# Kernel tuning notes

Hardware: AMD Instinct MI355X
Metric: run time of the kernel (lower is better)

## Reference

```python
import jax, jax.numpy as jnp
import numpy as np

HIDDEN = 1024
HEADS = 8
HEAD = HIDDEN // HEADS
EPS = 1e-5


def _gammas():
    lo = np.log(1.0 / 512.0)
    hi = np.log(1.0 / 32.0)
    lin = np.linspace(lo, hi, HEADS)
    return jnp.asarray(1.0 - np.exp(lin), dtype=jnp.float32)  # [H]


def setup_inputs() -> dict:
    key = jax.random.key(0)
    ks = jax.random.split(key, 7)
    B, S = 2, 2048
    x = jax.random.normal(ks[0], (B, S, HIDDEN), dtype=jnp.float32)
    # Per-head retention projection weights (Retention(head_size, gamma)): [H, d, d]
    Wq = jax.random.normal(ks[1], (HEADS, HEAD, HEAD), dtype=jnp.float32) / HEAD
    Wk = jax.random.normal(ks[2], (HEADS, HEAD, HEAD), dtype=jnp.float32) / HEAD
    Wv = jax.random.normal(ks[3], (HEADS, HEAD, HEAD), dtype=jnp.float32) / HEAD
    W1 = jax.random.normal(ks[4], (HIDDEN, HIDDEN), dtype=jnp.float32) / HIDDEN
    W2 = jax.random.normal(ks[5], (HIDDEN, HIDDEN), dtype=jnp.float32) / HIDDEN
    gn_w = jnp.ones((HIDDEN,), dtype=jnp.float32)
    gn_b = jnp.zeros((HIDDEN,), dtype=jnp.float32)
    return {"x": x, "Wq": Wq, "Wk": Wk, "Wv": Wv, "W1": W1, "W2": W2,
            "gn_w": gn_w, "gn_b": gn_b}


def _decay_mask(S, gammas):
    idx = jnp.arange(S)
    diff = idx[:, None] - idx[None, :]              # [S, S]
    causal = diff >= 0
    safe = jnp.where(causal, diff, 0).astype(jnp.float32)
    D = jnp.where(causal[None], gammas[:, None, None] ** safe[None], 0.0)  # [H,S,S]
    return D


def _msr_forward(x, Wq, Wk, Wv, W1, W2, gn_w, gn_b):
    B, S, _ = x.shape
    xh = x.reshape(B, S, HEADS, HEAD)               # per-head slices
    q = jnp.einsum('bshd,hde->bshe', xh, Wq)
    k = jnp.einsum('bshd,hde->bshe', xh, Wk)
    v = jnp.einsum('bshd,hde->bshe', xh, Wv)
    D = _decay_mask(S, _gammas())                   # [H,S,S]
    scores = jnp.einsum('bnhd,bmhd->bhnm', q, k) * D[None]
    ret = jnp.einsum('bhnm,bmhd->bnhd', scores, v)  # [B,S,H,d]
    # GroupNorm(num_groups=H, channels=HIDDEN) over flattened rows
    mu = jnp.mean(ret, axis=-1, keepdims=True)
    var = jnp.var(ret, axis=-1, keepdims=True)
    ret = (ret - mu) * jax.lax.rsqrt(var + EPS)
    ret = ret.reshape(B, S, HIDDEN) * gn_w + gn_b
    gated = x @ W1
    out = gated * jax.nn.sigmoid(gated) + ret       # swish gate + residual add
    return out @ W2


def reference(x, Wq, Wk, Wv, W1, W2, gn_w, gn_b):
    return _msr_forward(x, Wq, Wk, Wv, W1, W2, gn_w, gn_b)
```

## Files before the change

### kernel.cpp

```cpp
#include <hip/hip_runtime.h>
#include <hip/hip_bf16.h>

#define HID 1024
#define NH 8
#define HD 128
#define BB 2
#define SS 2048
#define CHK 128
#define NCH 16

typedef __attribute__((ext_vector_type(8))) short short8;
typedef __attribute__((ext_vector_type(4))) float f32x4;

static __device__ __forceinline__ float b2f(unsigned short u){
  unsigned int x = ((unsigned int)u) << 16; float f;
  __builtin_memcpy(&f, &x, 4); return f;
}
static __device__ __forceinline__ unsigned short f2b(float f){
  unsigned int x; __builtin_memcpy(&x, &f, 4);
  x += 0x7fffu + ((x >> 16) & 1u);
  return (unsigned short)(x >> 16);
}
static __device__ __forceinline__ float head_gamma(int h){
  double lo = -6.238324625039508;
  double hi = -3.4657359027997265;
  double lin = lo + (hi - lo) * ((double)h / 7.0);
  return (float)(1.0 - exp(lin));
}
static __device__ __forceinline__ f32x4 MFMA(short8 a, short8 b, f32x4 c){
  return __builtin_amdgcn_mfma_f32_16x16x32_bf16(a, b, c, 0, 0, 0);
}

typedef const __attribute__((address_space(1))) unsigned int* gas1_u32p;
typedef __attribute__((address_space(3))) unsigned int* las3_u32p;
static __device__ __forceinline__ void gload_lds16(const void* g, void* l){
  __builtin_amdgcn_global_load_lds((gas1_u32p)g, (las3_u32p)l, 16, 0, 0);
}

__global__ __launch_bounds__(256) void k_prep(
    const float* __restrict__ x,  unsigned short* __restrict__ xb,
    const float* __restrict__ W1, unsigned short* __restrict__ w1T,
    const float* __restrict__ W2, unsigned short* __restrict__ w2T,
    const float* __restrict__ Wq, unsigned short* __restrict__ wqT,
    const float* __restrict__ Wk, unsigned short* __restrict__ wkT,
    const float* __restrict__ Wv, unsigned short* __restrict__ wvT)
{
  int bid = blockIdx.x, t = threadIdx.x;
  if (bid < 1024){
    const int n = BB*SS*HID;
    int i = (bid*256 + t)*4;
    const int st = 1024*256*4;
    for (; i < n; i += st){
      float4 v = *(const float4*)(x + i);
      unsigned short o[4] = { f2b(v.x), f2b(v.y), f2b(v.z), f2b(v.w) };
      *(uint2*)(xb + i) = *(const uint2*)o;
    }
    return;
  }
  __shared__ float tile[32][33];
  const float* in; unsigned short* out; int R, C, r0, c0;
  if (bid < 3072){
    int which = (bid - 1024) >> 10;
    int local = (bid - 1024) & 1023;
    in  = which ? W2 : W1;  out = which ? w2T : w1T;
    R = C = HID;
    c0 = (local & 31)*32; r0 = (local >> 5)*32;
  } else {
    int local = bid - 3072;
    int mat = local >> 7;
    int rem = local & 127;
    int z = rem >> 4, tl2 = rem & 15;
    const float* ws[3] = { Wq, Wk, Wv };
    unsigned short* os[3] = { wqT, wkT, wvT };
    in  = ws[mat] + (size_t)z*HD*HD;
    out = os[mat] + (size_t)z*HD*HD;
    R = C = HD;
    c0 = (tl2 & 3)*32; r0 = (tl2 >> 2)*32;
  }
  int tx = t & 31, ty = t >> 5;
  #pragma unroll
  for (int i=0;i<4;i++) tile[ty+i*8][tx] = in[(size_t)(r0+ty+i*8)*C + c0+tx];
  __syncthreads();
  #pragma unroll
  for (int i=0;i<4;i++) out[(size_t)(c0+ty+i*8)*R + r0+tx] = f2b(tile[tx][ty+i*8]);
}

__global__ __launch_bounds__(256) void k_qkv(
    const unsigned short* __restrict__ xb,
    const unsigned short* __restrict__ wqT,
    const unsigned short* __restrict__ wkT,
    const unsigned short* __restrict__ wvT,
    unsigned short* __restrict__ qb,
    unsigned short* __restrict__ kb,
    unsigned short* __restrict__ ktsb,
    unsigned short* __restrict__ vtb)
{
  int bid = blockIdx.x;
  int stile = bid & 31;
  int bh = bid >> 5;
  int h = bh & 7, b = bh >> 3;
  int T0 = stile*64;
  int chunk = stile >> 1, pm0 = (stile & 1)*64;
  float l2g = log2f(head_gamma(h));
  __shared__ unsigned short tl[128*72];
  int t = threadIdx.x, wv = t>>6, l = t&63, lr = l&15, lg = l>>4;
  int row0 = T0 + wv*16;
  short8 a[4];
  const unsigned short* xp = xb + (size_t)(b*SS + row0 + lr)*HID + h*HD + lg*8;
  #pragma unroll
  for (int kk=0;kk<4;kk++) a[kk] = *(const short8*)(xp + kk*32);
  size_t obase = ((size_t)bh*SS + row0)*HD;
  size_t tbase = ((size_t)(bh*NCH + chunk))*HD*CHK + pm0;

  auto wout = [&](unsigned short* dst){
    int e = t & 127, th = t >> 7;
    const uint4* src = (const uint4*)(tl + e*72 + th*32);
    uint4* d4 = (uint4*)(dst + (size_t)e*CHK + th*32);
    #pragma unroll
    for (int i=0;i<4;i++) d4[i] = src[i];
  };

  {
    const unsigned short* wb = wqT + (size_t)h*HD*HD;
    unsigned short* op = qb + obase;
    #pragma unroll
    for (int nt=0;nt<8;nt++){
      f32x4 acc = {0.f,0.f,0.f,0.f};
      #pragma unroll
      for (int kk=0;kk<4;kk++){
        short8 bfr = *(const short8*)(wb + (size_t)(nt*16+lr)*HD + kk*32 + lg*8);
        acc = MFMA(a[kk], bfr, acc);
      }
      #pragma unroll
      for (int r=0;r<4;r++)
        op[(size_t)(lg*4+r)*HD + nt*16 + lr] = f2b(acc[r]);
    }
  }
  {
    const unsigned short* wb = wkT + (size_t)h*HD*HD;
    unsigned short* op = kb + obase;
    float ksc[4];
    #pragma unroll
    for (int r=0;r<4;r++)
      ksc[r] = exp2f((float)(127 - (pm0 + wv*16 + lg*4 + r))*l2g);
    #pragma unroll
    for (int nt=0;nt<8;nt++){
      f32x4 acc = {0.f,0.f,0.f,0.f};
      #pragma unroll
      for (int kk=0;kk<4;kk++){
        short8 bfr = *(const short8*)(wb + (size_t)(nt*16+lr)*HD + kk*32 + lg*8);
        acc = MFMA(a[kk], bfr, acc);
      }
      #pragma unroll
      for (int r=0;r<4;r++){
        op[(size_t)(lg*4+r)*HD + nt*16 + lr] = f2b(acc[r]);
        tl[(nt*16+lr)*72 + wv*16 + lg*4 + r] = f2b(acc[r]*ksc[r]);
      }
    }
  }
  __syncthreads();
  wout(ktsb + tbase);
  __syncthreads();
  {
    const unsigned short* wb = wvT + (size_t)h*HD*HD;
    #pragma unroll
    for (int nt=0;nt<8;nt++){
      f32x4 acc = {0.f,0.f,0.f,0.f};
      #pragma unroll
      for (int kk=0;kk<4;kk++){
        short8 bfr = *(const short8*)(wb + (size_t)(nt*16+lr)*HD + kk*32 + lg*8);
        acc = MFMA(a[kk], bfr, acc);
      }
      #pragma unroll
      for (int r=0;r<4;r++)
        tl[(nt*16+lr)*72 + wv*16 + lg*4 + r] = f2b(acc[r]);
    }
  }
  __syncthreads();
  wout(vtb + tbase);
}

__global__ __launch_bounds__(256) void k_sumscan(
    const unsigned short* __restrict__ ktsb,
    const unsigned short* __restrict__ vtb,
    unsigned short* __restrict__ ST)
{
  int bid = blockIdx.x;
  int dh = bid & 1, et = (bid >> 1) & 7, bh = bid >> 4;
  int h = bh & 7;
  float d128 = exp2f(128.f * log2f(head_gamma(h)));
  int t = threadIdx.x, wv = t>>6, l = t&63, lr = l&15, lg = l>>4;
  int e0 = et*16;
  int d0w = dh*64 + wv*16;
  const unsigned short* vt = vtb  + (size_t)bh*NCH*HD*CHK;
  const unsigned short* kt = ktsb + (size_t)bh*NCH*HD*CHK;
  unsigned short* Sb = ST + (size_t)bh*NCH*HD*HD;

  f32x4 s = {0.f,0.f,0.f,0.f};
  #pragma unroll
  for (int c=0;c<NCH;c++){
    const unsigned short* vc = vt + (size_t)c*HD*CHK;
    const unsigned short* kc = kt + (size_t)c*HD*CHK;
    f32x4 acc = {0.f,0.f,0.f,0.f};
    #pragma unroll
    for (int kk=0;kk<4;kk++){
      short8 af = *(const short8*)(vc + (size_t)(e0+lr)*CHK + kk*32 + lg*8);
      short8 bf = *(const short8*)(kc + (size_t)(d0w+lr)*CHK + kk*32 + lg*8);
      acc = MFMA(af, bf, acc);
    }
    unsigned short* So = Sb + (size_t)c*HD*HD;
    #pragma unroll
    for (int r=0;r<4;r++){
      So[(size_t)(e0+lg*4+r)*HD + d0w + lr] = f2b(s[r]);
      s[r] = s[r]*d128 + acc[r];
    }
  }
}

__global__ __launch_bounds__(256) void k_ret(
    const unsigned short* __restrict__ qb,
    const unsigned short* __restrict__ kb,
    const unsigned short* __restrict__ vtb,
    const unsigned short* __restrict__ ST,
    const float* __restrict__ gnw,
    const float* __restrict__ gnb,
    unsigned short* __restrict__ ret)
{
  int bid = blockIdx.x;
  int rh = bid & 1, cj = bid >> 1;
  int j = cj & 15, bh = cj >> 4, h = bh & 7, b = bh >> 3;
  int p = j*CHK, rbase = rh*64;
  float l2g = log2f(head_gamma(h));
  __shared__ unsigned short sc[64][136];
  int t = threadIdx.x, wv = t>>6, l = t&63, lr = l&15, lg = l>>4;
  const unsigned short* qc = qb + ((size_t)bh*SS + p)*HD;
  const unsigned short* kc = kb + ((size_t)bh*SS + p)*HD;
  const unsigned short* vt = vtb + (size_t)cj*HD*CHK;
  const unsigned short* Sp = ST + (size_t)cj*HD*HD;

  short8 qf[4];
  #pragma unroll
  for (int kk=0;kk<4;kk++)
    qf[kk] = *(const short8*)(qc + (size_t)(rbase + wv*16 + lr)*HD + kk*32 + lg*8);

  int ntmax = rh ? 8 : 4;
  for (int nt=0; nt<ntmax; nt++){
    f32x4 a0 = {0,0,0,0};
    #pragma unroll
    for (int kk=0;kk<4;kk++){
      short8 bfr = *(const short8*)(kc + (size_t)(nt*16+lr)*HD + kk*32 + lg*8);
      a0 = MFMA(qf[kk], bfr, a0);
    }
    int col = nt*16 + lr;
    #pragma unroll
    for (int r=0;r<4;r++){
      int n = rbase + wv*16 + lg*4 + r;
      float v0 = (col <= n) ? a0[r]*exp2f((float)(n-col)*l2g) : 0.f;
      sc[wv*16 + lg*4 + r][col] = f2b(v0);
    }
  }

  f32x4 acc[8];
  #pragma unroll
  for (int nt=0;nt<8;nt++){
    f32x4 aa = {0,0,0,0};
    #pragma unroll
    for (int kk=0;kk<4;kk++){
      short8 bfr = *(const short8*)(Sp + (size_t)(nt*16+lr)*HD + kk*32 + lg*8);
      aa = MFMA(qf[kk], bfr, aa);
    }
    acc[nt] = aa;
  }
  #pragma unroll
  for (int r=0;r<4;r++){
    int n = rbase + wv*16 + lg*4 + r;
    float sf = exp2f((float)(n+1)*l2g);
    #pragma unroll
    for (int nt=0;nt<8;nt++) acc[nt][r] *= sf;
  }

  int ksmax = rh ? 4 : 2;
  for (int ks=0; ks<ksmax; ks++){
    short8 afr = *(const short8*)&sc[wv*16 + lr][ks*32 + lg*8];
    #pragma unroll
    for (int nt=0;nt<8;nt++){
      short8 bfr = *(const short8*)(vt + (size_t)(nt*16+lr)*CHK + ks*32 + lg*8);
      acc[nt] = MFMA(afr, bfr, acc[nt]);
    }
  }

  unsigned short* rp = ret + ((size_t)(b*SS + p + rbase))*HID + h*HD;
  const float* gw  = gnw + h*HD;
  const float* gbb = gnb + h*HD;
  #pragma unroll
  for (int r=0;r<4;r++){
    float s = 0.f, ss = 0.f;
    #pragma unroll
    for (int nt=0;nt<8;nt++){ float x = acc[nt][r]; s += x; ss += x*x; }
    #pragma unroll
    for (int off=1; off<16; off<<=1){
      s  += __shfl_xor(s,  off, 64);
      ss += __shfl_xor(ss, off, 64);
    }
    float mu  = s*(1.f/128.f);
    float var = ss*(1.f/128.f) - mu*mu;
    float rs  = rsqrtf(var + 1e-5f);
    int lrow = wv*16 + lg*4 + r;
    unsigned short* orow = rp + (size_t)lrow*HID;
    #pragma unroll
    for (int nt=0;nt<8;nt++){
      int col = nt*16 + lr;
      orow[col] = f2b((acc[nt][r]-mu)*rs*gw[col] + gbb[col]);
    }
  }
}

template<int EPI>
__global__ __launch_bounds__(512) void k_gemm(
    const unsigned short* __restrict__ A,
    const unsigned short* __restrict__ BT,
    const unsigned short* __restrict__ radd,
    unsigned short* __restrict__ Cb,
    float* __restrict__ Cf,
    int M, int N, int K)
{
  __shared__ unsigned short ls[4][2][128*64];
  const int nb = N >> 7;
  const int nwg = (M >> 7) * nb;
  const int cpx = nwg >> 3;
  int bid0 = blockIdx.x;
  int bid = (bid0 & 7)*cpx + (bid0 >> 3);
  const int m0 = (bid / nb) << 7;
  const int n0 = (bid % nb) << 7;
  const int t = threadIdx.x, wv = t>>6, l = t&63, lr = l&15, lg = l>>4;
  const int wr = (wv>>1)<<5;
  const int wc = (wv&1)<<6;
  const int srow = l >> 3;
  const int sgc  = ((l & 7) ^ srow) << 3;
  const unsigned short* Abase = A  + (size_t)(m0 + wv*16 + srow)*K + sgc;
  const unsigned short* Bbase = BT + (size_t)(n0 + wv*16 + srow)*K + sgc;

  auto stage = [&](int buf, int kt){
    unsigned short* la = &ls[buf][0][0];
    unsigned short* lb = &ls[buf][1][0];
    int k0 = kt << 6;
    #pragma unroll
    for (int it=0; it<2; ++it){
      gload_lds16(Abase + (size_t)(it*8)*K + k0, la + (wv*16 + it*8)*64);
      gload_lds16(Bbase + (size_t)(it*8)*K + k0, lb + (wv*16 + it*8)*64);
    }
  };

  f32x4 acc[2][4];
  #pragma unroll
  for (int i=0;i<2;i++)
    #pragma unroll
    for (int j=0;j<4;j++) acc[i][j] = (f32x4){0,0,0,0};

  const int NT = K >> 6;
  stage(0,0); stage(1,1); stage(2,2);
  for (int kt = 0; kt < NT; ++kt){
    if (kt < NT-2)      asm volatile("s_waitcnt vmcnt(8)" ::: "memory");
    else if (kt == NT-2) asm volatile("s_waitcnt vmcnt(4)" ::: "memory");
    else                 asm volatile("s_waitcnt vmcnt(0)" ::: "memory");
    __builtin_amdgcn_s_barrier();
    __builtin_amdgcn_sched_barrier(0);
    if (kt+3 < NT) stage((kt+3)&3, kt+3);
    const unsigned short* pa = &ls[kt&3][0][0];
    const unsigned short* pb = &ls[kt&3][1][0];
    #pragma unroll
    for (int ks=0; ks<2; ++ks){
      short8 af[2], bf[4];
      #pragma unroll
      for (int i=0;i<2;i++){
        int ra = wr + i*16 + lr;
        af[i] = *(const short8*)(pa + ra*64 + ((((ks<<2)+lg) ^ (ra&7))<<3));
      }
      #pragma unroll
      for (int j=0;j<4;j++){
        int rb = wc + j*16 + lr;
        bf[j] = *(const short8*)(pb + rb*64 + ((((ks<<2)+lg) ^ (rb&7))<<3));
      }
      #pragma unroll
      for (int i=0;i<2;i++)
        #pragma unroll
        for (int j=0;j<4;j++)
          acc[i][j] = MFMA(af[i], bf[j], acc[i][j]);
    }
  }

  #pragma unroll
  for (int i=0;i<2;i++){
    #pragma unroll
    for (int j=0;j<4;j++){
      #pragma unroll
      for (int r=0;r<4;r++){
        int row = m0 + wr + i*16 + lg*4 + r;
        int col = n0 + wc + j*16 + lr;
        float v = acc[i][j][r];
        if (EPI == 1){
          float sw = v / (1.f + __expf(-v));
          Cb[(size_t)row*N + col] = f2b(sw + b2f(radd[(size_t)row*N + col]));
        } else {
          Cf[(size_t)row*N + col] = v;
        }
      }
    }
  }
}

extern "C" void kernel_launch(void* const* d_in, const int* in_sizes, int n_in,
                              void* d_out, int out_size, void* d_ws, size_t ws_size,
                              hipStream_t stream)
{
  (void)in_sizes; (void)n_in; (void)out_size; (void)ws_size;
  const float* x   = (const float*)d_in[0];
  const float* Wq  = (const float*)d_in[1];
  const float* Wk  = (const float*)d_in[2];
  const float* Wv  = (const float*)d_in[3];
  const float* W1  = (const float*)d_in[4];
  const float* W2  = (const float*)d_in[5];
  const float* gnw = (const float*)d_in[6];
  const float* gnb = (const float*)d_in[7];
  float* out = (float*)d_out;

  char* wsp = (char*)d_ws;
  size_t off = 0;
  auto alloc = [&](size_t bytes)->void*{
    off = (off + 255) & ~(size_t)255;
    void* p = wsp + off; off += bytes; return p;
  };
  const size_t NTOK = (size_t)BB*SS;
  unsigned short* xb   = (unsigned short*)alloc(NTOK*HID*2);
  unsigned short* w1T  = (unsigned short*)alloc((size_t)HID*HID*2);
  unsigned short* w2T  = (unsigned short*)alloc((size_t)HID*HID*2);
  unsigned short* wqT  = (unsigned short*)alloc((size_t)NH*HD*HD*2);
  unsigned short* wkT  = (unsigned short*)alloc((size_t)NH*HD*HD*2);
  unsigned short* wvT  = (unsigned short*)alloc((size_t)NH*HD*HD*2);
  unsigned short* qb   = (unsigned short*)alloc(NTOK*HID*2);
  unsigned short* kb   = (unsigned short*)alloc(NTOK*HID*2);
  unsigned short* ktsb = (unsigned short*)alloc(NTOK*HID*2);
  unsigned short* vtb  = (unsigned short*)alloc(NTOK*HID*2);
  unsigned short* ST   = (unsigned short*)alloc((size_t)BB*NH*NCH*HD*HD*2);
  unsigned short* rtb  = (unsigned short*)alloc(NTOK*HID*2);
  unsigned short* opb  = (unsigned short*)alloc(NTOK*HID*2);

  k_prep<<<dim3(3456), dim3(256), 0, stream>>>(x, xb, W1, w1T, W2, w2T,
                                               Wq, wqT, Wk, wkT, Wv, wvT);
  k_qkv<<<dim3(BB*NH*32), dim3(256), 0, stream>>>(xb, wqT, wkT, wvT, qb, kb, ktsb, vtb);
  k_sumscan<<<dim3(BB*NH*16), dim3(256), 0, stream>>>(ktsb, vtb, ST);
  k_ret<<<dim3(BB*NH*NCH*2), dim3(256), 0, stream>>>(qb, kb, vtb, ST, gnw, gnb, rtb);

  k_gemm<1><<<dim3(256), dim3(512), 0, stream>>>(xb,  w1T, rtb, opb, nullptr, (int)NTOK, HID, HID);
  k_gemm<2><<<dim3(256), dim3(512), 0, stream>>>(opb, w2T, nullptr, nullptr, out, (int)NTOK, HID, HID);
}
```

Measured before the change: 116.7 us.

## Retile output GEMMs to 64x128 double-buffered blocks; unroll retention loops fully

The two output GEMMs move from 128x128 tiles with 512 threads and a 4-stage async LDS pipeline to 64x128 tiles with 256 threads and a simple double buffer synchronised by __syncthreads. The grid doubles to 512 blocks. This is meant to improve occupancy and load balance across CUs, at the cost of shallower prefetch, more barrier stalls and less reuse per tile. In the retention kernel, the causal trip counts that depended on the row-half are replaced by fixed, fully unrolled loops. The lower row-half now does redundant masked work in exchange for straight-line code.

```diff
diff --git a/kernel.cpp b/kernel.cpp
--- a/kernel.cpp
+++ b/kernel.cpp
@@ -243,8 +243,8 @@
   for (int kk=0;kk<4;kk++)
     qf[kk] = *(const short8*)(qc + (size_t)(rbase + wv*16 + lr)*HD + kk*32 + lg*8);
 
-  int ntmax = rh ? 8 : 4;
-  for (int nt=0; nt<ntmax; nt++){
+  #pragma unroll
+  for (int nt=0; nt<8; nt++){
     f32x4 a0 = {0,0,0,0};
     #pragma unroll
     for (int kk=0;kk<4;kk++){
@@ -279,8 +279,8 @@
     for (int nt=0;nt<8;nt++) acc[nt][r] *= sf;
   }
 
-  int ksmax = rh ? 4 : 2;
-  for (int ks=0; ks<ksmax; ks++){
+  #pragma unroll
+  for (int ks=0; ks<4; ks++){
     short8 afr = *(const short8*)&sc[wv*16 + lr][ks*32 + lg*8];
     #pragma unroll
     for (int nt=0;nt<8;nt++){
@@ -316,7 +316,7 @@
 }
 
 template<int EPI>
-__global__ __launch_bounds__(512) void k_gemm(
+__global__ __launch_bounds__(256) void k_gemm(
     const unsigned short* __restrict__ A,
     const unsigned short* __restrict__ BT,
     const unsigned short* __restrict__ radd,
@@ -324,31 +324,30 @@
     float* __restrict__ Cf,
     int M, int N, int K)
 {
-  __shared__ unsigned short ls[4][2][128*64];
+  __shared__ unsigned short la[2][64*64];
+  __shared__ unsigned short lb[2][128*64];
   const int nb = N >> 7;
-  const int nwg = (M >> 7) * nb;
+  const int nwg = (M >> 6) * nb;
   const int cpx = nwg >> 3;
   int bid0 = blockIdx.x;
   int bid = (bid0 & 7)*cpx + (bid0 >> 3);
-  const int m0 = (bid / nb) << 7;
+  const int m0 = (bid / nb) << 6;
   const int n0 = (bid % nb) << 7;
   const int t = threadIdx.x, wv = t>>6, l = t&63, lr = l&15, lg = l>>4;
   const int wr = (wv>>1)<<5;
   const int wc = (wv&1)<<6;
   const int srow = l >> 3;
   const int sgc  = ((l & 7) ^ srow) << 3;
-  const unsigned short* Abase = A  + (size_t)(m0 + wv*16 + srow)*K + sgc;
-  const unsigned short* Bbase = BT + (size_t)(n0 + wv*16 + srow)*K + sgc;
-
-  auto stage = [&](int buf, int kt){
-    unsigned short* la = &ls[buf][0][0];
-    unsigned short* lb = &ls[buf][1][0];
-    int k0 = kt << 6;
-    #pragma unroll
-    for (int it=0; it<2; ++it){
-      gload_lds16(Abase + (size_t)(it*8)*K + k0, la + (wv*16 + it*8)*64);
-      gload_lds16(Bbase + (size_t)(it*8)*K + k0, lb + (wv*16 + it*8)*64);
-    }
+  const unsigned short* Ab = A  + (size_t)(m0 + wv*16 + srow)*K + sgc;
+  const unsigned short* Bb = BT + (size_t)(n0 + wv*32 + srow)*K + sgc;
+
+  auto stage = [&](int buf, int k0){
+    #pragma unroll
+    for (int it=0; it<2; ++it)
+      gload_lds16(Ab + (size_t)(it*8)*K + k0, &la[buf][(wv*16 + it*8)*64]);
+    #pragma unroll
+    for (int it=0; it<4; ++it)
+      gload_lds16(Bb + (size_t)(it*8)*K + k0, &lb[buf][(wv*32 + it*8)*64]);
   };
 
   f32x4 acc[2][4];
@@ -358,16 +357,13 @@
     for (int j=0;j<4;j++) acc[i][j] = (f32x4){0,0,0,0};
 
   const int NT = K >> 6;
-  stage(0,0); stage(1,1); stage(2,2);
+  stage(0, 0);
+  __syncthreads();
+  int cur = 0;
   for (int kt = 0; kt < NT; ++kt){
-    if (kt < NT-2)      asm volatile("s_waitcnt vmcnt(8)" ::: "memory");
-    else if (kt == NT-2) asm volatile("s_waitcnt vmcnt(4)" ::: "memory");
-    else                 asm volatile("s_waitcnt vmcnt(0)" ::: "memory");
-    __builtin_amdgcn_s_barrier();
-    __builtin_amdgcn_sched_barrier(0);
-    if (kt+3 < NT) stage((kt+3)&3, kt+3);
-    const unsigned short* pa = &ls[kt&3][0][0];
-    const unsigned short* pb = &ls[kt&3][1][0];
+    if (kt+1 < NT) stage(cur^1, (kt+1)<<6);
+    const unsigned short* pa = &la[cur][0];
+    const unsigned short* pb = &lb[cur][0];
     #pragma unroll
     for (int ks=0; ks<2; ++ks){
       short8 af[2], bf[4];
@@ -387,6 +383,8 @@
         for (int j=0;j<4;j++)
           acc[i][j] = MFMA(af[i], bf[j], acc[i][j]);
     }
+    __syncthreads();
+    cur ^= 1;
   }
 
   #pragma unroll
@@ -451,6 +449,6 @@
   k_sumscan<<<dim3(BB*NH*16), dim3(256), 0, stream>>>(ktsb, vtb, ST);
   k_ret<<<dim3(BB*NH*NCH*2), dim3(256), 0, stream>>>(qb, kb, vtb, ST, gnw, gnb, rtb);
 
-  k_gemm<1><<<dim3(256), dim3(512), 0, stream>>>(xb,  w1T, rtb, opb, nullptr, (int)NTOK, HID, HID);
-  k_gemm<2><<<dim3(256), dim3(512), 0, stream>>>(opb, w2T, nullptr, nullptr, out, (int)NTOK, HID, HID);
-}
+  k_gemm<1><<<dim3(512), dim3(256), 0, stream>>>(xb,  w1T, rtb, opb, nullptr, (int)NTOK, HID, HID);
+  k_gemm<2><<<dim3(512), dim3(256), 0, stream>>>(opb, w2T, nullptr, nullptr, out, (int)NTOK, HID, HID);
+}
```

New measurement: 122.6 us. +5.1%, slower.

## Fuse retention chunk computation into the W1 gate GEMM epilogue

Applied to the files above, without the earlier changes.

Merges the retention kernel into the x@W1 GEMM, so that each 128x128 output tile (one chunk of one head) computes the swish gate into shared memory and then computes the retention/GroupNorm for the same tile. The per-head retention output no longer goes to global memory and one launch is removed. In exchange, retention work now runs in 256 blocks of 8 waves instead of 512 blocks of 4, with uneven per-wave causal work and more register pressure in the fused kernel.

```diff
diff --git a/kernel.cpp b/kernel.cpp
--- a/kernel.cpp
+++ b/kernel.cpp
@@ -217,33 +217,116 @@
   }
 }
 
-__global__ __launch_bounds__(256) void k_ret(
+__global__ __launch_bounds__(512) void k_g1ret(
+    const unsigned short* __restrict__ A,
+    const unsigned short* __restrict__ BT,
     const unsigned short* __restrict__ qb,
     const unsigned short* __restrict__ kb,
     const unsigned short* __restrict__ vtb,
     const unsigned short* __restrict__ ST,
     const float* __restrict__ gnw,
     const float* __restrict__ gnb,
-    unsigned short* __restrict__ ret)
+    unsigned short* __restrict__ Cb,
+    int M, int N, int K)
 {
-  int bid = blockIdx.x;
-  int rh = bid & 1, cj = bid >> 1;
-  int j = cj & 15, bh = cj >> 4, h = bh & 7, b = bh >> 3;
-  int p = j*CHK, rbase = rh*64;
+  __shared__ unsigned short ls[4][2][128*64];
+  const int nb = N >> 7;
+  const int nwg = (M >> 7) * nb;
+  const int cpx = nwg >> 3;
+  int bid0 = blockIdx.x;
+  int bid = (bid0 & 7)*cpx + (bid0 >> 3);
+  const int m0 = (bid / nb) << 7;
+  const int n0 = (bid % nb) << 7;
+  const int t = threadIdx.x, wv = t>>6, l = t&63, lr = l&15, lg = l>>4;
+  const int wr = (wv>>1)<<5;
+  const int wc = (wv&1)<<6;
+  const int srow = l >> 3;
+  const int sgc  = ((l & 7) ^ srow) << 3;
+  const unsigned short* Abase = A  + (size_t)(m0 + wv*16 + srow)*K + sgc;
+  const unsigned short* Bbase = BT + (size_t)(n0 + wv*16 + srow)*K + sgc;
+
+  auto stage = [&](int buf, int kt){
+    unsigned short* la = &ls[buf][0][0];
+    unsigned short* lb = &ls[buf][1][0];
+    int k0 = kt << 6;
+    #pragma unroll
+    for (int it=0; it<2; ++it){
+      gload_lds16(Abase + (size_t)(it*8)*K + k0, la + (wv*16 + it*8)*64);
+      gload_lds16(Bbase + (size_t)(it*8)*K + k0, lb + (wv*16 + it*8)*64);
+    }
+  };
+
+  f32x4 acc[2][4];
+  #pragma unroll
+  for (int i=0;i<2;i++)
+    #pragma unroll
+    for (int j=0;j<4;j++) acc[i][j] = (f32x4){0,0,0,0};
+
+  const int NT = K >> 6;
+  stage(0,0); stage(1,1); stage(2,2);
+  for (int kt = 0; kt < NT; ++kt){
+    if (kt < NT-2)       asm volatile("s_waitcnt vmcnt(8)" ::: "memory");
+    else if (kt == NT-2) asm volatile("s_waitcnt vmcnt(4)" ::: "memory");
+    else                 asm volatile("s_waitcnt vmcnt(0)" ::: "memory");
+    __builtin_amdgcn_s_barrier();
+    __builtin_amdgcn_sched_barrier(0);
+    if (kt+3 < NT) stage((kt+3)&3, kt+3);
+    const unsigned short* pa = &ls[kt&3][0][0];
+    const unsigned short* pb = &ls[kt&3][1][0];
+    #pragma unroll
+    for (int ks=0; ks<2; ++ks){
+      short8 af[2], bf[4];
+      #pragma unroll
+      for (int i=0;i<2;i++){
+        int ra = wr + i*16 + lr;
+        af[i] = *(const short8*)(pa + ra*64 + ((((ks<<2)+lg) ^ (ra&7))<<3));
+      }
+      #pragma unroll
+      for (int j=0;j<4;j++){
+        int rb = wc + j*16 + lr;
+        bf[j] = *(const short8*)(pb + rb*64 + ((((ks<<2)+lg) ^ (rb&7))<<3));
+      }
+      #pragma unroll
+      for (int i=0;i<2;i++)
+        #pragma unroll
+        for (int j=0;j<4;j++)
+          acc[i][j] = MFMA(af[i], bf[j], acc[i][j]);
+    }
+  }
+  __syncthreads();
+
+  unsigned short* ct = (unsigned short*)&ls[0][0][0];
+  unsigned short* sc = ct + 128*136;
+  #pragma unroll
+  for (int i=0;i<2;i++){
+    #pragma unroll
+    for (int j=0;j<4;j++){
+      #pragma unroll
+      for (int r=0;r<4;r++){
+        int row = wr + i*16 + lg*4 + r;
+        int col = wc + j*16 + lr;
+        float v = acc[i][j][r];
+        ct[row*136 + col] = f2b(v / (1.f + __expf(-v)));
+      }
+    }
+  }
+  __syncthreads();
+
+  const int b = m0 >> 11, j = (m0 >> 7) & 15, h = n0 >> 7;
+  const int bh = b*NH + h;
+  const int cj = bh*NCH + j;
   float l2g = log2f(head_gamma(h));
-  __shared__ unsigned short sc[64][136];
-  int t = threadIdx.x, wv = t>>6, l = t&63, lr = l&15, lg = l>>4;
-  const unsigned short* qc = qb + ((size_t)bh*SS + p)*HD;
-  const unsigned short* kc = kb + ((size_t)bh*SS + p)*HD;
+  const unsigned short* qc = qb + ((size_t)bh*SS + j*CHK)*HD;
+  const unsigned short* kc = kb + ((size_t)bh*SS + j*CHK)*HD;
   const unsigned short* vt = vtb + (size_t)cj*HD*CHK;
   const unsigned short* Sp = ST + (size_t)cj*HD*HD;
 
   short8 qf[4];
   #pragma unroll
   for (int kk=0;kk<4;kk++)
-    qf[kk] = *(const short8*)(qc + (size_t)(rbase + wv*16 + lr)*HD + kk*32 + lg*8);
-
-  int ntmax = rh ? 8 : 4;
+    qf[kk] = *(const short8*)(qc + (size_t)(wv*16 + lr)*HD + kk*32 + lg*8);
+
+  int ntmax = (wv | 1) + 1;
   for (int nt=0; nt<ntmax; nt++){
     f32x4 a0 = {0,0,0,0};
     #pragma unroll
@@ -254,13 +337,13 @@
     int col = nt*16 + lr;
     #pragma unroll
     for (int r=0;r<4;r++){
-      int n = rbase + wv*16 + lg*4 + r;
+      int n = wv*16 + lg*4 + r;
       float v0 = (col <= n) ? a0[r]*exp2f((float)(n-col)*l2g) : 0.f;
-      sc[wv*16 + lg*4 + r][col] = f2b(v0);
-    }
-  }
-
-  f32x4 acc[8];
+      sc[(wv*16 + lg*4 + r)*136 + col] = f2b(v0);
+    }
+  }
+
+  f32x4 racc[8];
   #pragma unroll
   for (int nt=0;nt<8;nt++){
     f32x4 aa = {0,0,0,0};
@@ -269,34 +352,34 @@
       short8 bfr = *(const short8*)(Sp + (size_t)(nt*16+lr)*HD + kk*32 + lg*8);
       aa = MFMA(qf[kk], bfr, aa);
     }
-    acc[nt] = aa;
+    racc[nt] = aa;
   }
   #pragma unroll
   for (int r=0;r<4;r++){
-    int n = rbase + wv*16 + lg*4 + r;
+    int n = wv*16 + lg*4 + r;
     float sf = exp2f((float)(n+1)*l2g);
     #pragma unroll
-    for (int nt=0;nt<8;nt++) acc[nt][r] *= sf;
-  }
-
-  int ksmax = rh ? 4 : 2;
+    for (int nt=0;nt<8;nt++) racc[nt][r] *= sf;
+  }
+
+  int ksmax = (wv >> 1) + 1;
   for (int ks=0; ks<ksmax; ks++){
-    short8 afr = *(const short8*)&sc[wv*16 + lr][ks*32 + lg*8];
+    short8 afr = *(const short8*)&sc[(wv*16 + lr)*136 + ks*32 + lg*8];
     #pragma unroll
     for (int nt=0;nt<8;nt++){
       short8 bfr = *(const short8*)(vt + (size_t)(nt*16+lr)*CHK + ks*32 + lg*8);
-      acc[nt] = MFMA(afr, bfr, acc[nt]);
-    }
-  }
-
-  unsigned short* rp = ret + ((size_t)(b*SS + p + rbase))*HID + h*HD;
+      racc[nt] = MFMA(afr, bfr, racc[nt]);
+    }
+  }
+
+  unsigned short* op = Cb + (size_t)(m0 + wv*16)*N + n0;
   const float* gw  = gnw + h*HD;
   const float* gbb = gnb + h*HD;
   #pragma unroll
   for (int r=0;r<4;r++){
     float s = 0.f, ss = 0.f;
     #pragma unroll
-    for (int nt=0;nt<8;nt++){ float x = acc[nt][r]; s += x; ss += x*x; }
+    for (int nt=0;nt<8;nt++){ float x = racc[nt][r]; s += x; ss += x*x; }
     #pragma unroll
     for (int off=1; off<16; off<<=1){
       s  += __shfl_xor(s,  off, 64);
@@ -305,22 +388,20 @@
     float mu  = s*(1.f/128.f);
     float var = ss*(1.f/128.f) - mu*mu;
     float rs  = rsqrtf(var + 1e-5f);
-    int lrow = wv*16 + lg*4 + r;
-    unsigned short* orow = rp + (size_t)lrow*HID;
+    int lrow = lg*4 + r;
+    unsigned short* orow = op + (size_t)lrow*N;
     #pragma unroll
     for (int nt=0;nt<8;nt++){
       int col = nt*16 + lr;
-      orow[col] = f2b((acc[nt][r]-mu)*rs*gw[col] + gbb[col]);
-    }
-  }
-}
-
-template<int EPI>
-__global__ __launch_bounds__(512) void k_gemm(
+      float rv = (racc[nt][r]-mu)*rs*gw[col] + gbb[col];
+      orow[col] = f2b(rv + b2f(ct[(wv*16 + lrow)*136 + col]));
+    }
+  }
+}
+
+__global__ __launch_bounds__(512) void k_gemm2(
     const unsigned short* __restrict__ A,
     const unsigned short* __restrict__ BT,
-    const unsigned short* __restrict__ radd,
-    unsigned short* __restrict__ Cb,
     float* __restrict__ Cf,
     int M, int N, int K)
 {
@@ -360,7 +441,7 @@
   const int NT = K >> 6;
   stage(0,0); stage(1,1); stage(2,2);
   for (int kt = 0; kt < NT; ++kt){
-    if (kt < NT-2)      asm volatile("s_waitcnt vmcnt(8)" ::: "memory");
+    if (kt < NT-2)       asm volatile("s_waitcnt vmcnt(8)" ::: "memory");
     else if (kt == NT-2) asm volatile("s_waitcnt vmcnt(4)" ::: "memory");
     else                 asm volatile("s_waitcnt vmcnt(0)" ::: "memory");
     __builtin_amdgcn_s_barrier();
@@ -390,23 +471,15 @@
   }
 
   #pragma unroll
-  for (int i=0;i<2;i++){
-    #pragma unroll
-    for (int j=0;j<4;j++){
+  for (int i=0;i<2;i++)
+    #pragma unroll
+    for (int j=0;j<4;j++)
       #pragma unroll
       for (int r=0;r<4;r++){
         int row = m0 + wr + i*16 + lg*4 + r;
         int col = n0 + wc + j*16 + lr;
-        float v = acc[i][j][r];
-        if (EPI == 1){
-          float sw = v / (1.f + __expf(-v));
-          Cb[(size_t)row*N + col] = f2b(sw + b2f(radd[(size_t)row*N + col]));
-        } else {
-          Cf[(size_t)row*N + col] = v;
-        }
-      }
-    }
-  }
+        Cf[(size_t)row*N + col] = acc[i][j][r];
+      }
 }
 
 extern "C" void kernel_launch(void* const* d_in, const int* in_sizes, int n_in,
@@ -442,15 +515,14 @@
   unsigned short* ktsb = (unsigned short*)alloc(NTOK*HID*2);
   unsigned short* vtb  = (unsigned short*)alloc(NTOK*HID*2);
   unsigned short* ST   = (unsigned short*)alloc((size_t)BB*NH*NCH*HD*HD*2);
-  unsigned short* rtb  = (unsigned short*)alloc(NTOK*HID*2);
   unsigned short* opb  = (unsigned short*)alloc(NTOK*HID*2);
 
   k_prep<<<dim3(3456), dim3(256), 0, stream>>>(x, xb, W1, w1T, W2, w2T,
                                                Wq, wqT, Wk, wkT, Wv, wvT);
   k_qkv<<<dim3(BB*NH*32), dim3(256), 0, stream>>>(xb, wqT, wkT, wvT, qb, kb, ktsb, vtb);
   k_sumscan<<<dim3(BB*NH*16), dim3(256), 0, stream>>>(ktsb, vtb, ST);
-  k_ret<<<dim3(BB*NH*NCH*2), dim3(256), 0, stream>>>(qb, kb, vtb, ST, gnw, gnb, rtb);
-
-  k_gemm<1><<<dim3(256), dim3(512), 0, stream>>>(xb,  w1T, rtb, opb, nullptr, (int)NTOK, HID, HID);
-  k_gemm<2><<<dim3(256), dim3(512), 0, stream>>>(opb, w2T, nullptr, nullptr, out, (int)NTOK, HID, HID);
-}
+
+  k_g1ret<<<dim3(256), dim3(512), 0, stream>>>(xb, w1T, qb, kb, vtb, ST, gnw, gnb,
+                                               opb, (int)NTOK, HID, HID);
+  k_gemm2<<<dim3(256), dim3(512), 0, stream>>>(opb, w2T, out, (int)NTOK, HID, HID);
+}
```

Measured after the change: 111.2 us. -4.7%, faster.
